# Performance work log

Hardware: AMD Instinct MI355X
Metric: run time of the kernel (lower is better)

## Reference

```python
import jax, jax.numpy as jnp
import numpy as np
import math

DIM = 1024
MAX_DEPTH = 16
ROPE_BASE = 10000.0
NUM_ACTIVE = 2

def setup_inputs() -> dict:
    key = jax.random.key(0)
    ks = jax.random.split(key, 6)
    bsz, seq, dim, E, hidden = 4, 1024, DIM, 8, 4 * DIM
    bound = 1.0 / math.sqrt(dim)
    return {
        "x": jax.random.normal(ks[0], (bsz, seq, dim), jnp.float32),
        "router_w": jax.random.normal(ks[1], (dim, dim), jnp.float32) * 0.02,
        "expert_keys": jax.random.uniform(ks[2], (E, dim), jnp.float32, -bound, bound),
        "expert_bias": jnp.zeros((E,), jnp.float32),
        "fc_w": jax.random.normal(ks[3], (E, hidden, dim), jnp.float32) * 0.02,
        "proj_w": jax.random.normal(ks[4], (E, dim, hidden), jnp.float32) * 0.02,
        "depth_idx": 3,
    }

def _rope_row(depth_idx, rev_idx, dtype):
    half = DIM // 2
    inv_freq = 1.0 / (ROPE_BASE ** (jnp.arange(0, DIM, 2, dtype=jnp.float32) / DIM))  # [half]
    f = depth_idx * inv_freq
    r = rev_idx * inv_freq
    return (jnp.cos(f).astype(dtype), jnp.sin(f).astype(dtype),
            jnp.cos(r).astype(dtype), jnp.sin(r).astype(dtype))

def reference(x, router_w, expert_keys, expert_bias, fc_w, proj_w, depth_idx):
    bsz, seq, dim = x.shape
    N = bsz * seq
    flat_x = x.reshape(N, dim)
    # router + RMSNorm (no weight, eps = machine eps, matching F.rms_norm default)
    q = flat_x @ router_w.T
    eps = jnp.asarray(jnp.finfo(q.dtype).eps, q.dtype)
    q = q * jax.lax.rsqrt(jnp.mean(q * q, axis=-1, keepdims=True) + eps)
    # depth RoPE (forward freq on first half pairing, reverse freq on second half)
    half = dim // 2
    cos, sin, rcos, rsin = _rope_row(float(depth_idx), float(MAX_DEPTH - 1 - depth_idx), q.dtype)
    q1, q2 = q[..., :half], q[..., half:]
    q = jnp.concatenate((q1 * cos + q2 * sin, -q1 * rsin + q2 * rcos), axis=-1)
    # routing
    logits = (q @ expert_keys.T) / math.sqrt(dim)  # [N, E]
    gate_values = jax.nn.sigmoid(logits)
    biased = logits + expert_bias
    _, topk_idx = jax.lax.top_k(biased, NUM_ACTIVE)  # [N, k]
    topk_gates = jnp.take_along_axis(gate_values, topk_idx, axis=-1)
    topk_gates = topk_gates / jnp.clip(topk_gates.sum(-1, keepdims=True), 1e-9, None)
    gates = jnp.zeros_like(gate_values).at[jnp.arange(N)[:, None], topk_idx].set(topk_gates)
    # dense all-expert MLP: relu(x W_fc^T)^2 W_proj^T, then mask-and-sum
    h = jax.nn.relu(jnp.einsum('nd,ehd->neh', flat_x, fc_w))
    expert_out = jnp.einsum('neh,edh->ned', h * h, proj_w)  # [N, E, dim]
    y = jnp.einsum('ned,ne->nd', expert_out, gates)
    return y.reshape(bsz, seq, dim)
```

## Files before the change

kernel.cpp:

```cpp
#include <hip/hip_runtime.h>
#include <hip/hip_bf16.h>
#include <math.h>

#define N_TOK 4096
#define DIM_V 1024
#define NEXP  8
#define HID   4096
#define NSLOT 9216

typedef short  s16x8 __attribute__((ext_vector_type(8)));
typedef unsigned short u16x8 __attribute__((ext_vector_type(8)));
typedef unsigned short u16x4 __attribute__((ext_vector_type(4)));
typedef float  f32x4 __attribute__((ext_vector_type(4)));

constexpr size_t OFF_XB   = 0;
constexpr size_t OFF_WB   = OFF_XB + 8388608;
constexpr size_t OFF_RK   = OFF_WB + 2097152;
constexpr size_t OFF_KPP  = OFF_RK + 65536;
constexpr size_t OFF_SSQ  = OFF_KPP + 65536;
constexpr size_t OFF_CNT  = OFF_SSQ + 16384;
constexpr size_t OFF_CUR  = OFF_CNT + 128;
constexpr size_t OFF_TOK  = OFF_CUR + 128;
constexpr size_t OFF_GSL  = OFF_TOK + 36864;
constexpr size_t ZERO_BEG = OFF_KPP;
constexpr size_t ZERO_END = OFF_GSL + 36864;
constexpr size_t OFF_OFFP = ZERO_END;
constexpr size_t OFF_IDX2 = OFF_OFFP + 128;
constexpr size_t OFF_G2   = OFF_IDX2 + 32768;
constexpr size_t OFF_INV  = OFF_G2 + 32768;
constexpr size_t SMALL_END = OFF_INV + 32768;

constexpr size_t A_OFF_FCB = SMALL_END;
constexpr size_t A_OFF_PO  = A_OFF_FCB;
constexpr size_t A_OFF_PJB = A_OFF_FCB + 67108864;
constexpr size_t A_OFF_H2  = A_OFF_PJB + 67108864;
constexpr size_t WS_FULL   = A_OFF_H2 + 75497472;

__device__ inline unsigned short f2bf(float f) {
  __hip_bfloat16 h = __float2bfloat16(f);
  return __builtin_bit_cast(unsigned short, h);
}

__device__ __forceinline__ void gload16(const void* g, void* l) {
  __builtin_amdgcn_global_load_lds(
      (const __attribute__((address_space(1))) unsigned int*)g,
      (__attribute__((address_space(3))) unsigned int*)l, 16, 0, 0);
}

__global__ __launch_bounds__(256) void k_cvt_xw(
    const float* __restrict__ x, const float* __restrict__ rw,
    unsigned short* __restrict__ xb, unsigned short* __restrict__ wb) {
  int u = (int)blockIdx.x * 8;
  const f32x4* s; u16x4* d; int base;
  if (u < 1024) { s = (const f32x4*)x;  d = (u16x4*)xb; base = u; }
  else          { s = (const f32x4*)rw; d = (u16x4*)wb; base = u - 1024; }
  int j = base * 1024 + (int)threadIdx.x;
#pragma unroll 2
  for (int k = 0; k < 8; ++k, j += 1024) {
    f32x4 v0 = __builtin_nontemporal_load(s + j);
    f32x4 v1 = __builtin_nontemporal_load(s + j + 256);
    f32x4 v2 = __builtin_nontemporal_load(s + j + 512);
    f32x4 v3 = __builtin_nontemporal_load(s + j + 768);
    u16x4 o0 = { f2bf(v0.x), f2bf(v0.y), f2bf(v0.z), f2bf(v0.w) };
    u16x4 o1 = { f2bf(v1.x), f2bf(v1.y), f2bf(v1.z), f2bf(v1.w) };
    u16x4 o2 = { f2bf(v2.x), f2bf(v2.y), f2bf(v2.z), f2bf(v2.w) };
    u16x4 o3 = { f2bf(v3.x), f2bf(v3.y), f2bf(v3.z), f2bf(v3.w) };
    __builtin_nontemporal_store(o0, d + j);
    __builtin_nontemporal_store(o1, d + j + 256);
    __builtin_nontemporal_store(o2, d + j + 512);
    __builtin_nontemporal_store(o3, d + j + 768);
  }
}

constexpr int QTG = 256, CSG = 64, CVG = 2048;

__global__ __launch_bounds__(256) void k_mega(
    const unsigned short* __restrict__ xb, const unsigned short* __restrict__ wb,
    float* __restrict__ sumsq,
    const float* __restrict__ W, const float* __restrict__ keys,
    const int* __restrict__ depth, double* __restrict__ kpp,
    const float* __restrict__ fw, const float* __restrict__ pw,
    unsigned short* __restrict__ fcb, unsigned short* __restrict__ pjb) {
  __shared__ alignas(16) char smem[65536];
  const int bid = (int)blockIdx.x;
  const int tid = threadIdx.x;

  if (bid < QTG) {
    constexpr int KD = DIM_V, GNB = DIM_V / 128, NT = KD / 64, q = QTG >> 3;
    const int idp = (bid & 7) * q + (bid >> 3);
    const int n0 = (idp % GNB) * 128, m0 = (idp / GNB) * 128;
    const unsigned short* Bp = wb + (size_t)n0 * KD;
    const int wid = tid >> 6, lane = tid & 63;
    const int wr = (wid >> 1) * 64, wc = (wid & 1) * 64;
    const int rql  = tid >> 3;
    const int swc8 = ((tid & 7) ^ ((tid >> 3) & 7)) * 8;
    const int frow = lane & 15, fsl = lane >> 4, fkey = lane & 7;

    auto stage = [&](int k0s, unsigned db) {
#pragma unroll
      for (int p = 0; p < 4; ++p)
        gload16(xb + (size_t)(m0 + p * 32 + rql) * KD + k0s + swc8,
                smem + db + p * 4096 + wid * 1024);
#pragma unroll
      for (int p = 0; p < 4; ++p)
        gload16(Bp + (size_t)(p * 32 + rql) * KD + k0s + swc8,
                smem + db + 16384 + p * 4096 + wid * 1024);
    };

    f32x4 acc[4][4] = {};
    stage(0, 0);
#pragma unroll 2
    for (int t = 0; t < NT; ++t) {
      int tn = t + 1; if (tn == NT) tn = 0;
      stage(tn * 64, (unsigned)((t + 1) & 1) * 32768u);
      asm volatile("s_waitcnt vmcnt(8)" ::: "memory");
      __builtin_amdgcn_s_barrier();
      __builtin_amdgcn_sched_barrier(0);
      const unsigned Ab = (unsigned)(t & 1) * 32768u, Bb = Ab + 16384u;
      s16x8 af[2][4], bfr[2][4];
#pragma unroll
      for (int kk2 = 0; kk2 < 2; ++kk2) {
        const unsigned so = (unsigned)(((fsl + kk2 * 4) ^ fkey) << 4);
#pragma unroll
        for (int m = 0; m < 4; ++m)
          af[kk2][m] = *(const s16x8*)(smem + Ab + (unsigned)(wr + m * 16 + frow) * 128 + so);
#pragma unroll
        for (int n = 0; n < 4; ++n)
          bfr[kk2][n] = *(const s16x8*)(smem + Bb + (unsigned)(wc + n * 16 + frow) * 128 + so);
      }
      __builtin_amdgcn_s_setprio(1);
#pragma unroll
      for (int kk2 = 0; kk2 < 2; ++kk2)
#pragma unroll
        for (int m = 0; m < 4; ++m)
#pragma unroll
          for (int n = 0; n < 4; ++n)
            acc[m][n] = __builtin_amdgcn_mfma_f32_16x16x32_bf16(af[kk2][m], bfr[kk2][n],
                                                                acc[m][n], 0, 0, 0);
      __builtin_amdgcn_s_setprio(0);
      __builtin_amdgcn_sched_barrier(0);
      __builtin_amdgcn_s_barrier();
    }
#pragma unroll
    for (int m = 0; m < 4; ++m)
#pragma unroll
      for (int j = 0; j < 4; ++j) {
        const int grow = m0 + wr + m * 16 + (lane >> 4) * 4 + j;
        float s = 0.f;
#pragma unroll
        for (int n = 0; n < 4; ++n) { float v = acc[m][n][j]; s += v * v; }
        s += __shfl_xor(s, 1, 64); s += __shfl_xor(s, 2, 64);
        s += __shfl_xor(s, 4, 64); s += __shfl_xor(s, 8, 64);
        if ((lane & 15) == 0) atomicAdd(&sumsq[grow], s);
      }
  } else if (bid < QTG + CSG) {
    double (*rks)[64] = (double(*)[64])smem;
    const int cid = bid - QTG;
    const int d0 = (cid >> 2) * 64;
    if (tid < 64) {
      const int d = d0 + tid;
      const int dep = depth[0];
      const bool lower = d < 512;
      const int i = lower ? d : d - 512;
      double p = pow(10000.0, (double)i / 512.0);
      float invf = 1.0f / (float)p;
      float ff = (float)dep * invf;
      float rr = (float)(15 - dep) * invf;
      float cf  = (float)cos((double)ff);
      float sf  = (float)sin((double)ff);
      float rcf = (float)cos((double)rr);
      float rsf = (float)sin((double)rr);
      for (int e = 0; e < NEXP; ++e) {
        double k1 = (double)keys[e * DIM_V + i];
        double k2 = (double)keys[e * DIM_V + 512 + i];
        rks[e][tid] = lower ? ((double)cf * k1 - (double)rsf * k2)
                            : ((double)sf * k1 + (double)rcf * k2);
      }
    }
    __syncthreads();
    const int j = (cid & 3) * 256 + tid;
    double acc[NEXP] = {};
    for (int dd = 0; dd < 64; ++dd) {
      double w = (double)W[(size_t)(d0 + dd) * DIM_V + j];
#pragma unroll
      for (int e = 0; e < NEXP; ++e) acc[e] += w * rks[e][dd];
    }
    for (int e = 0; e < NEXP; ++e) atomicAdd(&kpp[e * DIM_V + j], acc[e]);
  } else {
    int u = (bid - QTG - CSG) * 8;
    const f32x4* s; u16x4* d; int base;
    if (u < 8192) { s = (const f32x4*)fw; d = (u16x4*)fcb; base = u; }
    else          { s = (const f32x4*)pw; d = (u16x4*)pjb; base = u - 8192; }
    int j = base * 1024 + tid;
#pragma unroll 2
    for (int k = 0; k < 8; ++k, j += 1024) {
      f32x4 v0 = __builtin_nontemporal_load(s + j);
      f32x4 v1 = __builtin_nontemporal_load(s + j + 256);
      f32x4 v2 = __builtin_nontemporal_load(s + j + 512);
      f32x4 v3 = __builtin_nontemporal_load(s + j + 768);
      u16x4 o0 = { f2bf(v0.x), f2bf(v0.y), f2bf(v0.z), f2bf(v0.w) };
      u16x4 o1 = { f2bf(v1.x), f2bf(v1.y), f2bf(v1.z), f2bf(v1.w) };
      u16x4 o2 = { f2bf(v2.x), f2bf(v2.y), f2bf(v2.z), f2bf(v2.w) };
      u16x4 o3 = { f2bf(v3.x), f2bf(v3.y), f2bf(v3.z), f2bf(v3.w) };
      __builtin_nontemporal_store(o0, d + j);
      __builtin_nontemporal_store(o1, d + j + 256);
      __builtin_nontemporal_store(o2, d + j + 512);
      __builtin_nontemporal_store(o3, d + j + 768);
    }
  }
}

__global__ __launch_bounds__(256) void k_gate(const float* __restrict__ x,
                                              const double* __restrict__ kpp,
                                              const float* __restrict__ sumsq,
                                              const float* __restrict__ bias,
                                              int* __restrict__ idx2, float* __restrict__ gates2,
                                              int* __restrict__ counts) {
  int wave = (blockIdx.x * 256 + threadIdx.x) >> 6;
  int lane = threadIdx.x & 63;
  if (wave >= N_TOK) return;
  const float4* xr = (const float4*)(x + (size_t)wave * DIM_V);
  double a[NEXP] = {};
#pragma unroll
  for (int j = 0; j < 4; ++j) {
    int c = lane + 64 * j;
    float4 v = xr[c];
#pragma unroll
    for (int e = 0; e < NEXP; ++e) {
      const double* kp = kpp + (size_t)e * DIM_V + c * 4;
      a[e] += (double)v.x * kp[0] + (double)v.y * kp[1] +
              (double)v.z * kp[2] + (double)v.w * kp[3];
    }
  }
#pragma unroll
  for (int e = 0; e < NEXP; ++e)
    for (int d = 1; d < 64; d <<= 1) a[e] += __shfl_xor(a[e], d, 64);
  if (lane == 0) {
    float s = rsqrtf(sumsq[wave] * (1.0f / 1024.0f) + 1.1920928955078125e-7f);
    float z[NEXP], b[NEXP];
#pragma unroll
    for (int e = 0; e < NEXP; ++e) {
      z[e] = (float)(a[e] * (double)s * (1.0 / 32.0));
      b[e] = z[e] + bias[e];
    }
    int i1 = 0;
    for (int e = 1; e < NEXP; ++e) if (b[e] > b[i1]) i1 = e;
    int i2 = -1;
    for (int e = 0; e < NEXP; ++e) if (e != i1 && (i2 < 0 || b[e] > b[i2])) i2 = e;
    float g1 = 1.f / (1.f + expf(-z[i1]));
    float g2 = 1.f / (1.f + expf(-z[i2]));
    float sm = fmaxf(g1 + g2, 1e-9f);
    idx2[wave * 2] = i1; idx2[wave * 2 + 1] = i2;
    gates2[wave * 2] = g1 / sm; gates2[wave * 2 + 1] = g2 / sm;
    atomicAdd(&counts[i1], 1); atomicAdd(&counts[i2], 1);
  }
}

__global__ void k_scatter(const int* __restrict__ idx2, const float* __restrict__ gates2,
                          const int* __restrict__ counts, int* __restrict__ cursor,
                          int* __restrict__ tok, float* __restrict__ gsl,
                          int* __restrict__ inv, int* __restrict__ offp_out) {
  int off[NEXP + 1];
  off[0] = 0;
  for (int e = 0; e < NEXP; ++e) off[e + 1] = off[e] + ((counts[e] + 127) & ~127);
  int n = blockIdx.x * 256 + threadIdx.x;
  if (blockIdx.x == 0 && threadIdx.x == 0)
    for (int e = 0; e <= NEXP; ++e) offp_out[e] = off[e];
  if (n >= N_TOK) return;
  for (int r = 0; r < 2; ++r) {
    int e = idx2[n * 2 + r];
    int pos = atomicAdd(&cursor[e], 1);
    int slot = off[e] + pos;
    tok[slot] = n; gsl[slot] = gates2[n * 2 + r]; inv[n * 2 + r] = slot;
  }
}

__global__ __launch_bounds__(512) void k_fc256(
    const unsigned short* __restrict__ xb,
    const unsigned short* __restrict__ fcb,
    const int* __restrict__ offp, const int* __restrict__ tok,
    unsigned short* __restrict__ h2) {
  constexpr int KD = DIM_V;
  constexpr int NT = KD / 64;
  const int G = gridDim.x, q = G >> 3;
  const int idp = ((int)blockIdx.x & 7) * q + ((int)blockIdx.x >> 3);
  const int bx = idp >> 4;
  const int n0 = (idp & 15) * 256;
  int c = 0, e = 0, m0 = -1;
  for (e = 0; e < NEXP; ++e) {
    int nb = (offp[e + 1] - offp[e] + 255) >> 8;
    if (bx < c + nb) { m0 = offp[e] + (bx - c) * 256; break; }
    c += nb;
  }
  if (m0 < 0) return;
  const int segend = offp[e + 1];
  const unsigned short* Bp = fcb + ((size_t)e * HID + n0) * KD;

  __shared__ alignas(16) char smem[131072];
  const int tid = threadIdx.x, wid = tid >> 6, lane = tid & 63;
  const int wr = (wid >> 2) * 128, wcc = (wid & 3) * 64;
  const int swc8 = ((tid & 7) ^ ((tid >> 3) & 7)) * 8;
  const int frow = lane & 15, fsl = lane >> 4, fkey = lane & 7;

  int arow[4];
#pragma unroll
  for (int p = 0; p < 4; ++p) {
    int rr = m0 + p * 64 + (tid >> 3);
    arow[p] = tok[rr < NSLOT ? rr : NSLOT - 1];
  }

  auto stage = [&](int k0s, unsigned db) {
#pragma unroll
    for (int p = 0; p < 4; ++p)
      gload16(xb + (size_t)arow[p] * KD + k0s + swc8,
              smem + db + p * 8192 + wid * 1024);
#pragma unroll
    for (int p = 0; p < 4; ++p)
      gload16(Bp + (size_t)(p * 64 + (tid >> 3)) * KD + k0s + swc8,
              smem + db + 32768 + p * 8192 + wid * 1024);
  };

  f32x4 acc[8][4] = {};
  stage(0, 0);
  for (int t = 0; t < NT; ++t) {
    int tn = t + 1; if (tn == NT) tn = 0;
    stage(tn * 64, (unsigned)((t + 1) & 1) * 65536u);
    asm volatile("s_waitcnt vmcnt(8)" ::: "memory");
    __builtin_amdgcn_s_barrier();
    __builtin_amdgcn_sched_barrier(0);
    const unsigned Ab = (unsigned)(t & 1) * 65536u, Bb = Ab + 32768u;
#pragma unroll
    for (int kk2 = 0; kk2 < 2; ++kk2) {
      const unsigned so = (unsigned)(((fsl + kk2 * 4) ^ fkey) << 4);
      s16x8 af[8], bfr[4];
#pragma unroll
      for (int m = 0; m < 8; ++m)
        af[m] = *(const s16x8*)(smem + Ab + (unsigned)(wr + m * 16 + frow) * 128 + so);
#pragma unroll
      for (int n = 0; n < 4; ++n)
        bfr[n] = *(const s16x8*)(smem + Bb + (unsigned)(wcc + n * 16 + frow) * 128 + so);
      __builtin_amdgcn_s_setprio(1);
#pragma unroll
      for (int m = 0; m < 8; ++m)
#pragma unroll
        for (int n = 0; n < 4; ++n)
          acc[m][n] = __builtin_amdgcn_mfma_f32_16x16x32_bf16(af[m], bfr[n], acc[m][n], 0, 0, 0);
      __builtin_amdgcn_s_setprio(0);
    }
    __builtin_amdgcn_sched_barrier(0);
    __builtin_amdgcn_s_barrier();
  }
#pragma unroll
  for (int m = 0; m < 8; ++m)
#pragma unroll
    for (int j = 0; j < 4; ++j) {
      const int grow = m0 + wr + m * 16 + (lane >> 4) * 4 + j;
      if (grow < segend) {
#pragma unroll
        for (int n = 0; n < 4; ++n) {
          float v = acc[m][n][j];
          v = v > 0.f ? v * v : 0.f;
          h2[(size_t)grow * HID + n0 + wcc + n * 16 + (lane & 15)] = f2bf(v);
        }
      }
    }
}

__global__ __launch_bounds__(256) void k_proj(
    const unsigned short* __restrict__ h2,
    const unsigned short* __restrict__ pjb,
    const int* __restrict__ offp, const float* __restrict__ gsl,
    float* __restrict__ po) {
  constexpr int KD  = HID;
  constexpr int GNB = DIM_V / 128;
  constexpr int NT  = KD / 64;
  const int G = gridDim.x, q = G >> 3;
  const int idp = ((int)blockIdx.x & 7) * q + ((int)blockIdx.x >> 3);
  const int n0 = (idp % GNB) * 128, m0 = (idp / GNB) * 128;
  if (m0 >= offp[NEXP]) return;
  int e = 0; while (e < NEXP - 1 && m0 >= offp[e + 1]) ++e;
  const unsigned short* Bp = pjb + ((size_t)e * DIM_V + n0) * KD;

  __shared__ alignas(16) char smem[65536];
  const int tid = threadIdx.x, wid = tid >> 6, lane = tid & 63;
  const int wr = (wid >> 1) * 64, wc = (wid & 1) * 64;
  const int rql  = tid >> 3;
  const int swc8 = ((tid & 7) ^ ((tid >> 3) & 7)) * 8;
  const int frow = lane & 15, fsl = lane >> 4, fkey = lane & 7;

  auto stage = [&](int k0s, unsigned db) {
#pragma unroll
    for (int p = 0; p < 4; ++p)
      gload16(h2 + (size_t)(m0 + p * 32 + rql) * KD + k0s + swc8,
              smem + db + p * 4096 + wid * 1024);
#pragma unroll
    for (int p = 0; p < 4; ++p)
      gload16(Bp + (size_t)(p * 32 + rql) * KD + k0s + swc8,
              smem + db + 16384 + p * 4096 + wid * 1024);
  };

  f32x4 acc[4][4] = {};
  stage(0, 0);
#pragma unroll 2
  for (int t = 0; t < NT; ++t) {
    int tn = t + 1; if (tn == NT) tn = 0;
    stage(tn * 64, (unsigned)((t + 1) & 1) * 32768u);
    asm volatile("s_waitcnt vmcnt(8)" ::: "memory");
    __builtin_amdgcn_s_barrier();
    __builtin_amdgcn_sched_barrier(0);
    const unsigned Ab = (unsigned)(t & 1) * 32768u, Bb = Ab + 16384u;
    s16x8 af[2][4], bfr[2][4];
#pragma unroll
    for (int kk2 = 0; kk2 < 2; ++kk2) {
      const unsigned so = (unsigned)(((fsl + kk2 * 4) ^ fkey) << 4);
#pragma unroll
      for (int m = 0; m < 4; ++m)
        af[kk2][m] = *(const s16x8*)(smem + Ab + (unsigned)(wr + m * 16 + frow) * 128 + so);
#pragma unroll
      for (int n = 0; n < 4; ++n)
        bfr[kk2][n] = *(const s16x8*)(smem + Bb + (unsigned)(wc + n * 16 + frow) * 128 + so);
    }
    __builtin_amdgcn_s_setprio(1);
#pragma unroll
    for (int kk2 = 0; kk2 < 2; ++kk2)
#pragma unroll
      for (int m = 0; m < 4; ++m)
#pragma unroll
        for (int n = 0; n < 4; ++n)
          acc[m][n] = __builtin_amdgcn_mfma_f32_16x16x32_bf16(af[kk2][m], bfr[kk2][n],
                                                              acc[m][n], 0, 0, 0);
    __builtin_amdgcn_s_setprio(0);
    __builtin_amdgcn_sched_barrier(0);
    __builtin_amdgcn_s_barrier();
  }

#pragma unroll
  for (int m = 0; m < 4; ++m)
#pragma unroll
    for (int j = 0; j < 4; ++j) {
      const int grow = m0 + wr + m * 16 + (lane >> 4) * 4 + j;
      const float g = gsl[grow];
#pragma unroll
      for (int n = 0; n < 4; ++n)
        po[(size_t)grow * DIM_V + n0 + wc + n * 16 + (lane & 15)] = acc[m][n][j] * g;
    }
}

__global__ void k_combine(const float* __restrict__ po, const int* __restrict__ inv,
                          float* __restrict__ y) {
  const int total = N_TOK * (DIM_V / 4);
  for (int i = blockIdx.x * blockDim.x + threadIdx.x; i < total;
       i += gridDim.x * blockDim.x) {
    int n = i >> 8, c = i & 255;
    int s1 = inv[n * 2], s2 = inv[n * 2 + 1];
    float4 a = ((const float4*)(po + (size_t)s1 * DIM_V))[c];
    float4 b = ((const float4*)(po + (size_t)s2 * DIM_V))[c];
    float4 o; o.x = a.x + b.x; o.y = a.y + b.y; o.z = a.z + b.z; o.w = a.w + b.w;
    ((float4*)(y + (size_t)n * DIM_V))[c] = o;
  }
}

extern "C" void kernel_launch(void* const* d_in, const int* in_sizes, int n_in,
                              void* d_out, int out_size, void* d_ws, size_t ws_size,
                              hipStream_t stream) {
  if (ws_size < WS_FULL) return;
  const float* x      = (const float*)d_in[0];
  const float* rw     = (const float*)d_in[1];
  const float* keys   = (const float*)d_in[2];
  const float* bias   = (const float*)d_in[3];
  const float* fc_w   = (const float*)d_in[4];
  const float* proj_w = (const float*)d_in[5];
  const int*   depth  = (const int*)d_in[6];
  char* ws = (char*)d_ws;
  unsigned short* xb  = (unsigned short*)(ws + OFF_XB);
  unsigned short* wb  = (unsigned short*)(ws + OFF_WB);
  double* kpp   = (double*)(ws + OFF_KPP);
  float*  ssq   = (float*)(ws + OFF_SSQ);
  int*    cnt   = (int*)(ws + OFF_CNT);
  int*    cur   = (int*)(ws + OFF_CUR);
  int*    tok   = (int*)(ws + OFF_TOK);
  float*  gsl   = (float*)(ws + OFF_GSL);
  int*    offp  = (int*)(ws + OFF_OFFP);
  int*    idx2  = (int*)(ws + OFF_IDX2);
  float*  g2    = (float*)(ws + OFF_G2);
  int*    inv   = (int*)(ws + OFF_INV);
  unsigned short* fcb = (unsigned short*)(ws + A_OFF_FCB);
  unsigned short* pjb = (unsigned short*)(ws + A_OFF_PJB);
  unsigned short* h2  = (unsigned short*)(ws + A_OFF_H2);
  float*  po    = (float*)(ws + A_OFF_PO);
  float*  y     = (float*)d_out;

  hipMemsetAsync(ws + ZERO_BEG, 0, ZERO_END - ZERO_BEG, stream);
  k_cvt_xw<<<160, 256, 0, stream>>>(x, rw, xb, wb);
  k_mega<<<QTG + CSG + CVG, 256, 0, stream>>>(xb, wb, ssq, rw, keys, depth, kpp,
                                              fc_w, proj_w, fcb, pjb);
  k_gate<<<1024, 256, 0, stream>>>(x, kpp, ssq, bias, idx2, g2, cnt);
  k_scatter<<<16, 256, 0, stream>>>(idx2, g2, cnt, cur, tok, gsl, inv, offp);
  k_fc256<<<dim3(44 * 16), 512, 0, stream>>>(xb, fcb, offp, tok, h2);
  k_proj<<<dim3(72 * 8), 256, 0, stream>>>(h2, pjb, offp, gsl, po);
  k_combine<<<2048, 256, 0, stream>>>(po, inv, y);
}
```

Baseline: 437.2 us.

## Fuse expert weight fp32-to-bf16 conversion into the fc and proj GEMM B-tile loads

Removes the separate pass in k_mega that converted all fc and proj expert weights to bf16 buffers in the workspace. The expert GEMMs now read fp32 weight tiles straight into registers, convert them to bf16 and write them into swizzled LDS. This drops a full write and re-read of the converted weight buffers and shrinks the workspace. In exchange, each GEMM block reads twice as many weight bytes, which are re-fetched by every M-tile of an expert. It also adds conversion ALU work and an extra barrier and full vmcnt wait per K-step.

```diff
diff --git a/kernel.cpp b/kernel.cpp
--- a/kernel.cpp
+++ b/kernel.cpp
@@ -15,8 +15,7 @@
 
 constexpr size_t OFF_XB   = 0;
 constexpr size_t OFF_WB   = OFF_XB + 8388608;
-constexpr size_t OFF_RK   = OFF_WB + 2097152;
-constexpr size_t OFF_KPP  = OFF_RK + 65536;
+constexpr size_t OFF_KPP  = OFF_WB + 2097152;
 constexpr size_t OFF_SSQ  = OFF_KPP + 65536;
 constexpr size_t OFF_CNT  = OFF_SSQ + 16384;
 constexpr size_t OFF_CUR  = OFF_CNT + 128;
@@ -30,11 +29,9 @@
 constexpr size_t OFF_INV  = OFF_G2 + 32768;
 constexpr size_t SMALL_END = OFF_INV + 32768;
 
-constexpr size_t A_OFF_FCB = SMALL_END;
-constexpr size_t A_OFF_PO  = A_OFF_FCB;
-constexpr size_t A_OFF_PJB = A_OFF_FCB + 67108864;
-constexpr size_t A_OFF_H2  = A_OFF_PJB + 67108864;
-constexpr size_t WS_FULL   = A_OFF_H2 + 75497472;
+constexpr size_t A_OFF_H2  = SMALL_END;
+constexpr size_t A_OFF_PO  = A_OFF_H2 + 75497472;
+constexpr size_t WS_NEED   = A_OFF_PO + 37748736;
 
 __device__ inline unsigned short f2bf(float f) {
   __hip_bfloat16 h = __float2bfloat16(f);
@@ -72,15 +69,13 @@
   }
 }
 
-constexpr int QTG = 256, CSG = 64, CVG = 2048;
+constexpr int QTG = 256, CSG = 64;
 
 __global__ __launch_bounds__(256) void k_mega(
     const unsigned short* __restrict__ xb, const unsigned short* __restrict__ wb,
     float* __restrict__ sumsq,
     const float* __restrict__ W, const float* __restrict__ keys,
-    const int* __restrict__ depth, double* __restrict__ kpp,
-    const float* __restrict__ fw, const float* __restrict__ pw,
-    unsigned short* __restrict__ fcb, unsigned short* __restrict__ pjb) {
+    const int* __restrict__ depth, double* __restrict__ kpp) {
   __shared__ alignas(16) char smem[65536];
   const int bid = (int)blockIdx.x;
   const int tid = threadIdx.x;
@@ -153,7 +148,7 @@
         s += __shfl_xor(s, 4, 64); s += __shfl_xor(s, 8, 64);
         if ((lane & 15) == 0) atomicAdd(&sumsq[grow], s);
       }
-  } else if (bid < QTG + CSG) {
+  } else {
     double (*rks)[64] = (double(*)[64])smem;
     const int cid = bid - QTG;
     const int d0 = (cid >> 2) * 64;
@@ -186,27 +181,6 @@
       for (int e = 0; e < NEXP; ++e) acc[e] += w * rks[e][dd];
     }
     for (int e = 0; e < NEXP; ++e) atomicAdd(&kpp[e * DIM_V + j], acc[e]);
-  } else {
-    int u = (bid - QTG - CSG) * 8;
-    const f32x4* s; u16x4* d; int base;
-    if (u < 8192) { s = (const f32x4*)fw; d = (u16x4*)fcb; base = u; }
-    else          { s = (const f32x4*)pw; d = (u16x4*)pjb; base = u - 8192; }
-    int j = base * 1024 + tid;
-#pragma unroll 2
-    for (int k = 0; k < 8; ++k, j += 1024) {
-      f32x4 v0 = __builtin_nontemporal_load(s + j);
-      f32x4 v1 = __builtin_nontemporal_load(s + j + 256);
-      f32x4 v2 = __builtin_nontemporal_load(s + j + 512);
-      f32x4 v3 = __builtin_nontemporal_load(s + j + 768);
-      u16x4 o0 = { f2bf(v0.x), f2bf(v0.y), f2bf(v0.z), f2bf(v0.w) };
-      u16x4 o1 = { f2bf(v1.x), f2bf(v1.y), f2bf(v1.z), f2bf(v1.w) };
-      u16x4 o2 = { f2bf(v2.x), f2bf(v2.y), f2bf(v2.z), f2bf(v2.w) };
-      u16x4 o3 = { f2bf(v3.x), f2bf(v3.y), f2bf(v3.z), f2bf(v3.w) };
-      __builtin_nontemporal_store(o0, d + j);
-      __builtin_nontemporal_store(o1, d + j + 256);
-      __builtin_nontemporal_store(o2, d + j + 512);
-      __builtin_nontemporal_store(o3, d + j + 768);
-    }
   }
 }
 
@@ -277,7 +251,7 @@
 
 __global__ __launch_bounds__(512) void k_fc256(
     const unsigned short* __restrict__ xb,
-    const unsigned short* __restrict__ fcb,
+    const float* __restrict__ fw,
     const int* __restrict__ offp, const int* __restrict__ tok,
     unsigned short* __restrict__ h2) {
   constexpr int KD = DIM_V;
@@ -294,13 +268,16 @@
   }
   if (m0 < 0) return;
   const int segend = offp[e + 1];
-  const unsigned short* Bp = fcb + ((size_t)e * HID + n0) * KD;
 
   __shared__ alignas(16) char smem[131072];
   const int tid = threadIdx.x, wid = tid >> 6, lane = tid & 63;
   const int wr = (wid >> 2) * 128, wcc = (wid & 3) * 64;
   const int swc8 = ((tid & 7) ^ ((tid >> 3) & 7)) * 8;
   const int frow = lane & 15, fsl = lane >> 4, fkey = lane & 7;
+  const int brow = tid >> 1, bhalf = tid & 1;
+  const float* Bsrc = fw + ((size_t)e * HID + n0 + brow) * KD + bhalf * 32;
+  const unsigned bwslot = (unsigned)brow * 128u
+                        + (unsigned)(((bhalf * 4 + 0) ^ (brow & 7)) * 16);
 
   int arow[4];
 #pragma unroll
@@ -309,24 +286,49 @@
     arow[p] = tok[rr < NSLOT ? rr : NSLOT - 1];
   }
 
-  auto stage = [&](int k0s, unsigned db) {
+  auto stageA = [&](int k0s, unsigned db) {
 #pragma unroll
     for (int p = 0; p < 4; ++p)
       gload16(xb + (size_t)arow[p] * KD + k0s + swc8,
               smem + db + p * 8192 + wid * 1024);
-#pragma unroll
-    for (int p = 0; p < 4; ++p)
-      gload16(Bp + (size_t)(p * 64 + (tid >> 3)) * KD + k0s + swc8,
-              smem + db + 32768 + p * 8192 + wid * 1024);
   };
 
+  f32x4 breg[8];
+  auto loadB = [&](int k0s) {
+    const f32x4* sp = (const f32x4*)(Bsrc + k0s);
+#pragma unroll
+    for (int qq = 0; qq < 4; ++qq) {
+      breg[2 * qq]     = sp[2 * qq];
+      breg[2 * qq + 1] = sp[2 * qq + 1];
+    }
+#pragma unroll
+    for (int r = 0; r < 8; ++r)
+      asm volatile("" :: "v"(breg[r]));
+  };
+  auto writeB = [&](unsigned db) {
+#pragma unroll
+    for (int qq = 0; qq < 4; ++qq) {
+      f32x4 a = breg[2 * qq], b = breg[2 * qq + 1];
+      u16x8 o = { f2bf(a.x), f2bf(a.y), f2bf(a.z), f2bf(a.w),
+                  f2bf(b.x), f2bf(b.y), f2bf(b.z), f2bf(b.w) };
+      unsigned sl = (unsigned)(((bhalf * 4 + qq) ^ (brow & 7)) * 16);
+      *(u16x8*)(smem + db + 32768u + (unsigned)brow * 128u + sl) = o;
+    }
+  };
+
+  stageA(0, 0);
+  loadB(0);
+  asm volatile("s_waitcnt vmcnt(0)" ::: "memory");
+  writeB(0);
+  asm volatile("s_waitcnt lgkmcnt(0)" ::: "memory");
+  __builtin_amdgcn_s_barrier();
+
   f32x4 acc[8][4] = {};
-  stage(0, 0);
   for (int t = 0; t < NT; ++t) {
     int tn = t + 1; if (tn == NT) tn = 0;
-    stage(tn * 64, (unsigned)((t + 1) & 1) * 65536u);
-    asm volatile("s_waitcnt vmcnt(8)" ::: "memory");
-    __builtin_amdgcn_s_barrier();
+    const unsigned dbn = (unsigned)((t + 1) & 1) * 65536u;
+    stageA(tn * 64, dbn);
+    loadB(tn * 64);
     __builtin_amdgcn_sched_barrier(0);
     const unsigned Ab = (unsigned)(t & 1) * 65536u, Bb = Ab + 32768u;
 #pragma unroll
@@ -348,6 +350,10 @@
       __builtin_amdgcn_s_setprio(0);
     }
     __builtin_amdgcn_sched_barrier(0);
+    __builtin_amdgcn_s_barrier();
+    asm volatile("s_waitcnt vmcnt(0)" ::: "memory");
+    writeB(dbn);
+    asm volatile("s_waitcnt lgkmcnt(0)" ::: "memory");
     __builtin_amdgcn_s_barrier();
   }
 #pragma unroll
@@ -368,7 +374,7 @@
 
 __global__ __launch_bounds__(256) void k_proj(
     const unsigned short* __restrict__ h2,
-    const unsigned short* __restrict__ pjb,
+    const float* __restrict__ pw,
     const int* __restrict__ offp, const float* __restrict__ gsl,
     float* __restrict__ po) {
   constexpr int KD  = HID;
@@ -379,7 +385,6 @@
   const int n0 = (idp % GNB) * 128, m0 = (idp / GNB) * 128;
   if (m0 >= offp[NEXP]) return;
   int e = 0; while (e < NEXP - 1 && m0 >= offp[e + 1]) ++e;
-  const unsigned short* Bp = pjb + ((size_t)e * DIM_V + n0) * KD;
 
   __shared__ alignas(16) char smem[65536];
   const int tid = threadIdx.x, wid = tid >> 6, lane = tid & 63;
@@ -387,26 +392,52 @@
   const int rql  = tid >> 3;
   const int swc8 = ((tid & 7) ^ ((tid >> 3) & 7)) * 8;
   const int frow = lane & 15, fsl = lane >> 4, fkey = lane & 7;
-
-  auto stage = [&](int k0s, unsigned db) {
+  const int brow = tid >> 1, bhalf = tid & 1;
+  const float* Bsrc = pw + ((size_t)e * DIM_V + n0 + brow) * KD + bhalf * 32;
+
+  auto stageA = [&](int k0s, unsigned db) {
 #pragma unroll
     for (int p = 0; p < 4; ++p)
       gload16(h2 + (size_t)(m0 + p * 32 + rql) * KD + k0s + swc8,
               smem + db + p * 4096 + wid * 1024);
-#pragma unroll
-    for (int p = 0; p < 4; ++p)
-      gload16(Bp + (size_t)(p * 32 + rql) * KD + k0s + swc8,
-              smem + db + 16384 + p * 4096 + wid * 1024);
   };
 
+  f32x4 breg[8];
+  auto loadB = [&](int k0s) {
+    const f32x4* sp = (const f32x4*)(Bsrc + k0s);
+#pragma unroll
+    for (int qq = 0; qq < 4; ++qq) {
+      breg[2 * qq]     = sp[2 * qq];
+      breg[2 * qq + 1] = sp[2 * qq + 1];
+    }
+#pragma unroll
+    for (int r = 0; r < 8; ++r)
+      asm volatile("" :: "v"(breg[r]));
+  };
+  auto writeB = [&](unsigned db) {
+#pragma unroll
+    for (int qq = 0; qq < 4; ++qq) {
+      f32x4 a = breg[2 * qq], b = breg[2 * qq + 1];
+      u16x8 o = { f2bf(a.x), f2bf(a.y), f2bf(a.z), f2bf(a.w),
+                  f2bf(b.x), f2bf(b.y), f2bf(b.z), f2bf(b.w) };
+      unsigned sl = (unsigned)(((bhalf * 4 + qq) ^ (brow & 7)) * 16);
+      *(u16x8*)(smem + db + 16384u + (unsigned)brow * 128u + sl) = o;
+    }
+  };
+
+  stageA(0, 0);
+  loadB(0);
+  asm volatile("s_waitcnt vmcnt(0)" ::: "memory");
+  writeB(0);
+  asm volatile("s_waitcnt lgkmcnt(0)" ::: "memory");
+  __builtin_amdgcn_s_barrier();
+
   f32x4 acc[4][4] = {};
-  stage(0, 0);
-#pragma unroll 2
   for (int t = 0; t < NT; ++t) {
     int tn = t + 1; if (tn == NT) tn = 0;
-    stage(tn * 64, (unsigned)((t + 1) & 1) * 32768u);
-    asm volatile("s_waitcnt vmcnt(8)" ::: "memory");
-    __builtin_amdgcn_s_barrier();
+    const unsigned dbn = (unsigned)((t + 1) & 1) * 32768u;
+    stageA(tn * 64, dbn);
+    loadB(tn * 64);
     __builtin_amdgcn_sched_barrier(0);
     const unsigned Ab = (unsigned)(t & 1) * 32768u, Bb = Ab + 16384u;
     s16x8 af[2][4], bfr[2][4];
@@ -431,6 +462,10 @@
                                                               acc[m][n], 0, 0, 0);
     __builtin_amdgcn_s_setprio(0);
     __builtin_amdgcn_sched_barrier(0);
+    __builtin_amdgcn_s_barrier();
+    asm volatile("s_waitcnt vmcnt(0)" ::: "memory");
+    writeB(dbn);
+    asm volatile("s_waitcnt lgkmcnt(0)" ::: "memory");
     __builtin_amdgcn_s_barrier();
   }
 
@@ -463,7 +498,7 @@
 extern "C" void kernel_launch(void* const* d_in, const int* in_sizes, int n_in,
                               void* d_out, int out_size, void* d_ws, size_t ws_size,
                               hipStream_t stream) {
-  if (ws_size < WS_FULL) return;
+  if (ws_size < WS_NEED) return;
   const float* x      = (const float*)d_in[0];
   const float* rw     = (const float*)d_in[1];
   const float* keys   = (const float*)d_in[2];
@@ -484,19 +519,16 @@
   int*    idx2  = (int*)(ws + OFF_IDX2);
   float*  g2    = (float*)(ws + OFF_G2);
   int*    inv   = (int*)(ws + OFF_INV);
-  unsigned short* fcb = (unsigned short*)(ws + A_OFF_FCB);
-  unsigned short* pjb = (unsigned short*)(ws + A_OFF_PJB);
   unsigned short* h2  = (unsigned short*)(ws + A_OFF_H2);
   float*  po    = (float*)(ws + A_OFF_PO);
   float*  y     = (float*)d_out;
 
   hipMemsetAsync(ws + ZERO_BEG, 0, ZERO_END - ZERO_BEG, stream);
   k_cvt_xw<<<160, 256, 0, stream>>>(x, rw, xb, wb);
-  k_mega<<<QTG + CSG + CVG, 256, 0, stream>>>(xb, wb, ssq, rw, keys, depth, kpp,
-                                              fc_w, proj_w, fcb, pjb);
+  k_mega<<<QTG + CSG, 256, 0, stream>>>(xb, wb, ssq, rw, keys, depth, kpp);
   k_gate<<<1024, 256, 0, stream>>>(x, kpp, ssq, bias, idx2, g2, cnt);
   k_scatter<<<16, 256, 0, stream>>>(idx2, g2, cnt, cur, tok, gsl, inv, offp);
-  k_fc256<<<dim3(44 * 16), 512, 0, stream>>>(xb, fcb, offp, tok, h2);
-  k_proj<<<dim3(72 * 8), 256, 0, stream>>>(h2, pjb, offp, gsl, po);
+  k_fc256<<<dim3(44 * 16), 512, 0, stream>>>(xb, fc_w, offp, tok, h2);
+  k_proj<<<dim3(72 * 8), 256, 0, stream>>>(h2, proj_w, offp, gsl, po);
   k_combine<<<2048, 256, 0, stream>>>(po, inv, y);
 }
```

Result: slower. 719.8 us (+64.6%).
